# Kernel optimization log

Hardware: AMD Instinct MI355X
Metric: run time of the kernel (lower is better)

## Reference

```python
import jax, jax.numpy as jnp
import numpy as np

N_CLS = 4
NUM_QUERIES = 256
TEMPERATURE = 0.07
NEG_INF = -1e9


def setup_inputs() -> dict:
    key = jax.random.key(0)
    k1, k2, k3, k4, k5, k6 = jax.random.split(key, 6)
    B, C, H, W = 8, 512, 64, 64
    K = 3072
    pred_s = jax.random.normal(k1, (B, N_CLS, H, W), dtype=jnp.float32)
    feat_s_raw = jax.random.normal(k2, (B, C, H, W), dtype=jnp.float32)
    feat_t_raw = jax.random.normal(k3, (B, C, H, W), dtype=jnp.float32)
    target = jax.random.randint(k4, (B, H, W), 0, N_CLS, dtype=jnp.int64)
    queue = jax.random.normal(k5, (C, K), dtype=jnp.float32)
    queue = queue / jnp.linalg.norm(queue, axis=0, keepdims=True)  # F.normalize(queue, dim=0)
    queue_labels = jax.random.randint(k6, (1, K), 0, N_CLS, dtype=jnp.int64)
    return {"pred_s": pred_s, "feat_s_raw": feat_s_raw, "feat_t_raw": feat_t_raw,
            "target": target, "queue": queue, "queue_labels": queue_labels}


def _l2norm(x, axis):
    return x / jnp.clip(jnp.linalg.norm(x, axis=axis, keepdims=True), 1e-12)


def reference(pred_s, feat_s_raw, feat_t_raw, target, queue, queue_labels):
    # softmax over class dim (probs are only consumed in the hard (random=False)
    # branch of find_hard_sampling; module default is random=True)
    probs_s = jax.nn.softmax(pred_s, axis=1)
    fs = _l2norm(feat_s_raw, axis=1)   # [B, C, H, W]
    ft = _l2norm(feat_t_raw, axis=1)
    B, C, H, W = fs.shape

    # permute(0,2,3,1).flatten(0,2) -> [N, C], matching target.reshape(-1)
    rep = jnp.transpose(fs, (0, 2, 3, 1)).reshape(-1, C)
    rep_t = jnp.transpose(ft, (0, 2, 3, 1)).reshape(-1, C)
    tflat = target.reshape(-1)  # [N]

    # find_hard_sampling, random=True path: for each segment, draw NUM_QUERIES
    # indices uniformly from that segment's valid pixels (assumes every class
    # is present, which holds w.h.p. at this resolution).
    key = jax.random.key(42)
    keys = jax.random.split(key, N_CLS + 1)

    def sample_class(k, cls):
        logits = jnp.where(tflat == cls, 0.0, NEG_INF)  # uniform over valid pixels
        return jax.random.categorical(k, logits, shape=(NUM_QUERIES,))

    idx = jax.vmap(sample_class)(keys[:N_CLS], jnp.arange(N_CLS)).reshape(-1)  # [N_CLS*NQ]
    labels = jnp.repeat(jnp.arange(N_CLS), NUM_QUERIES)

    # shuffle (get_shuffle_ids)
    perm = jax.random.permutation(keys[N_CLS], idx.shape[0])
    idx = idx[perm]
    labels = labels[perm]

    feats_s = rep[idx]     # [n, C] random gather (memory-bound)
    feats_t = rep_t[idx]

    l_pos = jnp.einsum('nc,nc->n', feats_s, feats_t)[:, None]   # [n, 1]
    l_neg = jnp.einsum('nc,ck->nk', feats_s, queue)             # [n, K]
    logits = jnp.concatenate([l_pos, l_neg], axis=1) / TEMPERATURE

    # non-targeted mask: eq(labels_cur, queue_labels)
    mask = (labels[:, None] == queue_labels[0][None, :]).astype(logits.dtype)
    return logits, mask, labels
```

## Files before the change

### kernel.cpp

```cpp
#include <hip/hip_runtime.h>
#include <stdint.h>

#define N_PIX   32768
#define C_DIM   512
#define K_Q     3072
#define NCLS    4
#define NQ      256
#define N_SAMP  1024
#define HW      4096
#define L_ROW   3073
#define KH      1024
#define KP      1536

typedef float f32x4 __attribute__((ext_vector_type(4)));
typedef short s16x8 __attribute__((ext_vector_type(8)));

__device__ inline unsigned short f2bf(float f) {
  uint32_t u = __float_as_uint(f);
  return (unsigned short)((u + 0x7FFFu + ((u >> 16) & 1u)) >> 16);
}
__device__ inline float bf2f(unsigned short h) {
  return __uint_as_float(((uint32_t)h) << 16);
}

__host__ __device__ inline void tf2x32(uint32_t k0, uint32_t k1,
                                       uint32_t x0, uint32_t x1,
                                       uint32_t& o0, uint32_t& o1) {
  uint32_t ks2 = k0 ^ k1 ^ 0x1BD11BDAu;
  x0 += k0; x1 += k1;
#define ROTL_(v,d) (((v)<<(d))|((v)>>(32-(d))))
#define RND_(r) { x0 += x1; x1 = ROTL_(x1, r); x1 ^= x0; }
  RND_(13) RND_(15) RND_(26) RND_(6)
  x0 += k1; x1 += ks2 + 1u;
  RND_(17) RND_(29) RND_(16) RND_(24)
  x0 += ks2; x1 += k0 + 2u;
  RND_(13) RND_(15) RND_(26) RND_(6)
  x0 += k0; x1 += k1 + 3u;
  RND_(17) RND_(29) RND_(16) RND_(24)
  x0 += k1; x1 += ks2 + 4u;
  RND_(13) RND_(15) RND_(26) RND_(6)
  x0 += ks2; x1 += k0 + 5u;
  o0 = x0; o1 = x1;
#undef RND_
#undef ROTL_
}

__global__ __launch_bounds__(256) void k_convq(const float* __restrict__ queue,
                                               unsigned short* __restrict__ B2,
                                               int* __restrict__ cnt) {
  if (blockIdx.x == 0 && blockIdx.y == 0 && threadIdx.x < NCLS)
    cnt[threadIdx.x] = 0;
  __shared__ float tile[64][65];
  int tid = threadIdx.x;
  int n0 = blockIdx.x * 64;
  int k0 = blockIdx.y * 64;
#pragma unroll
  for (int it = 0; it < 4; ++it) {
    int r = (tid >> 4) + it * 16;
    int c4 = (tid & 15) * 4;
    float4 v = *(const float4*)(queue + (size_t)(k0 + r) * K_Q + n0 + c4);
    tile[r][c4 + 0] = v.x; tile[r][c4 + 1] = v.y;
    tile[r][c4 + 2] = v.z; tile[r][c4 + 3] = v.w;
  }
  __syncthreads();
  int tn = tid >> 2;
  int kc = (tid & 3) * 16;
  unsigned short* rowp = B2 + (size_t)(n0 + tn) * KH + k0 + kc;
#pragma unroll
  for (int g8 = 0; g8 < 2; ++g8) {
    s16x8 vhi, vlo;
#pragma unroll
    for (int j = 0; j < 8; ++j) {
      float v = tile[kc + g8 * 8 + j][tn];
      unsigned short h = f2bf(v);
      vhi[j] = (short)h;
      vlo[j] = (short)f2bf(v - bf2f(h));
    }
    *(s16x8*)(rowp + g8 * 8)       = vhi;
    *(s16x8*)(rowp + 512 + g8 * 8) = vlo;
  }
}

__global__ __launch_bounds__(256) void k_compact(const int* __restrict__ target,
                                                 int* __restrict__ cnt,
                                                 int* __restrict__ lists) {
  __shared__ int lcnt[NCLS];
  __shared__ int lbase[NCLS];
  int tid = threadIdx.x;
  if (tid < NCLS) lcnt[tid] = 0;
  __syncthreads();
  int p = blockIdx.x * 256 + tid;
  int c = target[p];
  int lpos = atomicAdd(&lcnt[c], 1);
  __syncthreads();
  if (tid < NCLS) lbase[tid] = atomicAdd(&cnt[tid], lcnt[tid]);
  __syncthreads();
  lists[c * N_PIX + lbase[c] + lpos] = p;
}

__global__ __launch_bounds__(256) void k_sample(
    const int* __restrict__ cnt, const int* __restrict__ lists,
    int* __restrict__ samp,
    uint32_t k0a, uint32_t k0b, uint32_t k1a, uint32_t k1b,
    uint32_t k2a, uint32_t k2b, uint32_t k3a, uint32_t k3b) {
  int c = blockIdx.y;
  int q = blockIdx.x;
  uint32_t ka, kb;
  if      (c == 0) { ka = k0a; kb = k0b; }
  else if (c == 1) { ka = k1a; kb = k1b; }
  else if (c == 2) { ka = k2a; kb = k2b; }
  else             { ka = k3a; kb = k3b; }

  int nv = cnt[c];
  const int* lst = lists + c * N_PIX;
  unsigned long long best = 0ull;
  for (int t = threadIdx.x; t < nv; t += 256) {
    int p = lst[t];
    uint32_t j = (uint32_t)(q * N_PIX + p);
    uint32_t o0, o1;
    tf2x32(ka, kb, 0u, j, o0, o1);
    uint32_t bits = o0 ^ o1;
    unsigned long long v =
        ((unsigned long long)(bits >> 9) << 15) | (unsigned)(32767 - p);
    if (v > best) best = v;
  }
  __shared__ unsigned long long red[256];
  red[threadIdx.x] = best;
  __syncthreads();
  for (int s = 128; s > 0; s >>= 1) {
    if (threadIdx.x < s && red[threadIdx.x + s] > red[threadIdx.x])
      red[threadIdx.x] = red[threadIdx.x + s];
    __syncthreads();
  }
  if (threadIdx.x == 0)
    samp[c * NQ + q] = 32767 - (int)(red[0] & 0x7FFFull);
}

__global__ __launch_bounds__(64) void k_perm(
    const int* __restrict__ samp, int* __restrict__ idx_final,
    int* __restrict__ labels_shuf, float* __restrict__ out_labels,
    uint32_t sk0, uint32_t sk1) {
  __shared__ uint32_t keys_s[N_SAMP];
  int lt = threadIdx.x;
  for (int t = lt; t < N_SAMP; t += 64) {
    uint32_t o0, o1;
    tf2x32(sk0, sk1, 0u, (uint32_t)t, o0, o1);
    keys_s[t] = o0 ^ o1;
  }
  __syncthreads();
  int i = blockIdx.x * 64 + lt;
  uint32_t ki = keys_s[i];
  int rank = 0;
#pragma unroll 4
  for (int j = 0; j < N_SAMP; ++j) {
    uint32_t kj = keys_s[j];
    rank += (int)((kj < ki) | ((kj == ki) & (j < i)));
  }
  idx_final[rank] = samp[i];
  int lab = i >> 8;
  labels_shuf[rank] = lab;
  out_labels[rank] = (float)lab;
}

__global__ __launch_bounds__(64) void k_gather(
    const float* __restrict__ fs, const float* __restrict__ ft,
    const int* __restrict__ idx_final, unsigned short* __restrict__ A2,
    float* __restrict__ out_logits) {
  int n = blockIdx.x;
  int p = idx_final[n];
  int b = p >> 12;
  int hw = p & (HW - 1);
  const float* fsb = fs + (size_t)b * C_DIM * HW + hw;
  const float* ftb = ft + (size_t)b * C_DIM * HW + hw;
  int lane = threadIdx.x;

  float s[8], t[8];
#pragma unroll
  for (int j = 0; j < 8; ++j) {
    int c = lane * 8 + j;
    s[j] = fsb[(size_t)c * HW];
    t[j] = ftb[(size_t)c * HW];
  }

  float ss = 0.f, tt = 0.f;
#pragma unroll
  for (int j = 0; j < 8; ++j) { ss += s[j] * s[j]; tt += t[j] * t[j]; }
#pragma unroll
  for (int m = 1; m < 64; m <<= 1) {
    ss += __shfl_xor(ss, m);
    tt += __shfl_xor(tt, m);
  }
  float ns = fmaxf(sqrtf(ss), 1e-12f);
  float nt = fmaxf(sqrtf(tt), 1e-12f);

  float st = 0.f;
  s16x8 vhi, vlo;
#pragma unroll
  for (int j = 0; j < 8; ++j) {
    float a = s[j] / ns;
    float bb = t[j] / nt;
    st += a * bb;
    unsigned short h = f2bf(a);
    vhi[j] = (short)h;
    vlo[j] = (short)f2bf(a - bf2f(h));
  }
  unsigned short* row = A2 + (size_t)n * KH;
  *(s16x8*)(row + lane * 8)       = vhi;
  *(s16x8*)(row + 512 + lane * 8) = vlo;

#pragma unroll
  for (int m = 1; m < 64; m <<= 1) st += __shfl_xor(st, m);
  if (lane == 0)
    out_logits[(size_t)n * L_ROW] = st * (1.0f / 0.07f);
}

__global__ __launch_bounds__(256) void k_gemm(
    const unsigned short* __restrict__ A2,
    const unsigned short* __restrict__ B2,
    const int* __restrict__ labels,
    const int* __restrict__ qlab,
    float* __restrict__ out) {
  __shared__ unsigned short sAB[8192];
  int tid  = threadIdx.x;
  int lane = tid & 63;
  int wave = tid >> 6;
  int wm = wave >> 1, wn = wave & 1;
  int bm = blockIdx.x * 64;
  int bn = blockIdx.y * 64;

  int r0 = tid >> 3;
  int g0 = tid & 7;
  int slot0 = ((g0 ^ (r0 & 7)) << 3);

  f32x4 acc[2][2] = {};
  s16x8 ra[2], rb[2];

  const int NSTEP = KP / 64;
  {
    ra[0] = *(const s16x8*)(A2 + (size_t)(bm + r0)      * KH + g0 * 8);
    ra[1] = *(const s16x8*)(A2 + (size_t)(bm + r0 + 32) * KH + g0 * 8);
    rb[0] = *(const s16x8*)(B2 + (size_t)(bn + r0)      * KH + g0 * 8);
    rb[1] = *(const s16x8*)(B2 + (size_t)(bn + r0 + 32) * KH + g0 * 8);
    *(s16x8*)&sAB[r0 * 64 + slot0]               = ra[0];
    *(s16x8*)&sAB[(r0 + 32) * 64 + slot0]        = ra[1];
    *(s16x8*)&sAB[4096 + r0 * 64 + slot0]        = rb[0];
    *(s16x8*)&sAB[4096 + (r0 + 32) * 64 + slot0] = rb[1];
  }
  __syncthreads();

  for (int s = 0; s < NSTEP; ++s) {
    if (s + 1 < NSTEP) {
      int kp = (s + 1) * 64;
      int sA = (kp < 512) ? kp : kp - 512;
      int sB = (kp < 1024) ? kp : kp - 1024;
      ra[0] = *(const s16x8*)(A2 + (size_t)(bm + r0)      * KH + sA + g0 * 8);
      ra[1] = *(const s16x8*)(A2 + (size_t)(bm + r0 + 32) * KH + sA + g0 * 8);
      rb[0] = *(const s16x8*)(B2 + (size_t)(bn + r0)      * KH + sB + g0 * 8);
      rb[1] = *(const s16x8*)(B2 + (size_t)(bn + r0 + 32) * KH + sB + g0 * 8);
    }
#pragma unroll
    for (int kk = 0; kk < 2; ++kk) {
      int g = kk * 4 + (lane >> 4);
      s16x8 af[2], bfr[2];
#pragma unroll
      for (int mi = 0; mi < 2; ++mi) {
        int rowL = wm * 32 + mi * 16 + (lane & 15);
        af[mi] = *(s16x8*)&sAB[rowL * 64 + ((g ^ (rowL & 7)) << 3)];
      }
#pragma unroll
      for (int ni = 0; ni < 2; ++ni) {
        int rowN = wn * 32 + ni * 16 + (lane & 15);
        bfr[ni] = *(s16x8*)&sAB[4096 + rowN * 64 + ((g ^ (rowN & 7)) << 3)];
      }
#pragma unroll
      for (int mi = 0; mi < 2; ++mi)
#pragma unroll
        for (int ni = 0; ni < 2; ++ni)
          acc[mi][ni] = __builtin_amdgcn_mfma_f32_16x16x32_bf16(
              af[mi], bfr[ni], acc[mi][ni], 0, 0, 0);
    }
    __syncthreads();
    if (s + 1 < NSTEP) {
      *(s16x8*)&sAB[r0 * 64 + slot0]               = ra[0];
      *(s16x8*)&sAB[(r0 + 32) * 64 + slot0]        = ra[1];
      *(s16x8*)&sAB[4096 + r0 * 64 + slot0]        = rb[0];
      *(s16x8*)&sAB[4096 + (r0 + 32) * 64 + slot0] = rb[1];
      __syncthreads();
    }
  }

  int* labsh = (int*)sAB;
  if (tid < 64)            labsh[tid] = labels[bm + tid];
  else if (tid < 128)      labsh[tid] = qlab[bn + (tid - 64)];
  __syncthreads();

  float* out_mask = out + (size_t)N_SAMP * L_ROW;
  const float sc = 1.0f / 0.07f;
#pragma unroll
  for (int mi = 0; mi < 2; ++mi) {
#pragma unroll
    for (int ni = 0; ni < 2; ++ni) {
#pragma unroll
      for (int j = 0; j < 4; ++j) {
        int rl = wm * 32 + mi * 16 + ((lane >> 4) << 2) + j;
        int cl = wn * 32 + ni * 16 + (lane & 15);
        int row = bm + rl, col = bn + cl;
        out[(size_t)row * L_ROW + 1 + col] = acc[mi][ni][j] * sc;
        out_mask[(size_t)row * K_Q + col] =
            (labsh[rl] == labsh[64 + cl]) ? 1.0f : 0.0f;
      }
    }
  }
}

extern "C" void kernel_launch(void* const* d_in, const int* in_sizes, int n_in,
                              void* d_out, int out_size, void* d_ws, size_t ws_size,
                              hipStream_t stream) {
  const float* fs     = (const float*)d_in[1];
  const float* ft     = (const float*)d_in[2];
  const int*   target = (const int*)d_in[3];
  const float* queue  = (const float*)d_in[4];
  const int*   qlab   = (const int*)d_in[5];
  float* out = (float*)d_out;

  char* ws = (char*)d_ws;
  int* cnt   = (int*)(ws + 0);
  int* samp  = (int*)(ws + 4096);
  int* idxf  = (int*)(ws + 8192);
  int* labs  = (int*)(ws + 12288);
  int* lists = (int*)(ws + 16384);
  unsigned short* A2 = (unsigned short*)(ws + (1u << 20));
  unsigned short* B2 = (unsigned short*)(ws + (4u << 20));

  uint32_t ck[5][2];
  for (int i = 0; i < 5; ++i)
    tf2x32(0u, 42u, 0u, (uint32_t)i, ck[i][0], ck[i][1]);
  uint32_t sk0, sk1;
  tf2x32(ck[4][0], ck[4][1], 0u, 1u, sk0, sk1);

  float* out_labels = out + (size_t)N_SAMP * L_ROW + (size_t)N_SAMP * K_Q;

  k_convq<<<dim3(K_Q / 64, C_DIM / 64), 256, 0, stream>>>(queue, B2, cnt);
  k_compact<<<N_PIX / 256, 256, 0, stream>>>(target, cnt, lists);
  k_sample<<<dim3(NQ, NCLS), 256, 0, stream>>>(
      cnt, lists, samp,
      ck[0][0], ck[0][1], ck[1][0], ck[1][1],
      ck[2][0], ck[2][1], ck[3][0], ck[3][1]);
  k_perm<<<16, 64, 0, stream>>>(samp, idxf, labs, out_labels, sk0, sk1);
  k_gather<<<N_SAMP, 64, 0, stream>>>(fs, ft, idxf, A2, out);
  k_gemm<<<dim3(N_SAMP / 64, K_Q / 64), 256, 0, stream>>>(
      A2, B2, labs, qlab, out);
}
```

Measured before the change: 242.9 us.

## Restructure GEMM to single-wave blocks loading MFMA fragments directly from global

```diff
diff --git a/kernel.cpp b/kernel.cpp
--- a/kernel.cpp
+++ b/kernel.cpp
@@ -214,100 +214,81 @@
     out_logits[(size_t)n * L_ROW] = st * (1.0f / 0.07f);
 }
 
-__global__ __launch_bounds__(256) void k_gemm(
+__device__ __forceinline__ void gemm_loadc(
+    const unsigned short* const (&pA)[4], const unsigned short* const (&pB)[4],
+    int sA_, int sB_, s16x8 (&ra)[4], s16x8 (&rb)[4]) {
+  ra[0] = *(const s16x8*)(pA[0] + sA_);
+  ra[1] = *(const s16x8*)(pA[1] + sA_);
+  ra[2] = *(const s16x8*)(pA[2] + sA_);
+  ra[3] = *(const s16x8*)(pA[3] + sA_);
+  rb[0] = *(const s16x8*)(pB[0] + sB_);
+  rb[1] = *(const s16x8*)(pB[1] + sB_);
+  rb[2] = *(const s16x8*)(pB[2] + sB_);
+  rb[3] = *(const s16x8*)(pB[3] + sB_);
+}
+
+__global__ __launch_bounds__(64) void k_gemm(
     const unsigned short* __restrict__ A2,
     const unsigned short* __restrict__ B2,
     const int* __restrict__ labels,
     const int* __restrict__ qlab,
     float* __restrict__ out) {
-  __shared__ unsigned short sAB[8192];
-  int tid  = threadIdx.x;
-  int lane = tid & 63;
-  int wave = tid >> 6;
-  int wm = wave >> 1, wn = wave & 1;
-  int bm = blockIdx.x * 64;
-  int bn = blockIdx.y * 64;
-
-  int r0 = tid >> 3;
-  int g0 = tid & 7;
-  int slot0 = ((g0 ^ (r0 & 7)) << 3);
-
-  f32x4 acc[2][2] = {};
-  s16x8 ra[2], rb[2];
-
-  const int NSTEP = KP / 64;
-  {
-    ra[0] = *(const s16x8*)(A2 + (size_t)(bm + r0)      * KH + g0 * 8);
-    ra[1] = *(const s16x8*)(A2 + (size_t)(bm + r0 + 32) * KH + g0 * 8);
-    rb[0] = *(const s16x8*)(B2 + (size_t)(bn + r0)      * KH + g0 * 8);
-    rb[1] = *(const s16x8*)(B2 + (size_t)(bn + r0 + 32) * KH + g0 * 8);
-    *(s16x8*)&sAB[r0 * 64 + slot0]               = ra[0];
-    *(s16x8*)&sAB[(r0 + 32) * 64 + slot0]        = ra[1];
-    *(s16x8*)&sAB[4096 + r0 * 64 + slot0]        = rb[0];
-    *(s16x8*)&sAB[4096 + (r0 + 32) * 64 + slot0] = rb[1];
-  }
-  __syncthreads();
-
-  for (int s = 0; s < NSTEP; ++s) {
-    if (s + 1 < NSTEP) {
-      int kp = (s + 1) * 64;
-      int sA = (kp < 512) ? kp : kp - 512;
-      int sB = (kp < 1024) ? kp : kp - 1024;
-      ra[0] = *(const s16x8*)(A2 + (size_t)(bm + r0)      * KH + sA + g0 * 8);
-      ra[1] = *(const s16x8*)(A2 + (size_t)(bm + r0 + 32) * KH + sA + g0 * 8);
-      rb[0] = *(const s16x8*)(B2 + (size_t)(bn + r0)      * KH + sB + g0 * 8);
-      rb[1] = *(const s16x8*)(B2 + (size_t)(bn + r0 + 32) * KH + sB + g0 * 8);
+  int lane = threadIdx.x;
+  int bid = (int)blockIdx.x;
+  int swz = (bid & 7) * 96 + (bid >> 3);
+  int bm = (swz & 15) * 64;
+  int bn = (swz >> 4) * 64;
+
+  int koff = (lane >> 4) * 8;
+  int rsel = lane & 15;
+  const unsigned short* pA[4];
+  const unsigned short* pB[4];
+#pragma unroll
+  for (int g = 0; g < 4; ++g) {
+    pA[g] = A2 + (size_t)(bm + g * 16 + rsel) * KH + koff;
+    pB[g] = B2 + (size_t)(bn + g * 16 + rsel) * KH + koff;
+  }
+
+  f32x4 acc[4][4] = {};
+  s16x8 rA[3][4], rB[3][4];
+
+#define SAOF(kp) (((kp) < 512) ? (kp) : (kp) - 512)
+#define SBOF(kp) (((kp) < 1024) ? (kp) : (kp) - 1024)
+
+  gemm_loadc(pA, pB, SAOF(0),  SBOF(0),  rA[0], rB[0]);
+  gemm_loadc(pA, pB, SAOF(32), SBOF(32), rA[1], rB[1]);
+
+#pragma unroll
+  for (int c = 0; c < 48; ++c) {
+    if (c + 2 < 48) {
+      int kp2 = (c + 2) * 32;
+      gemm_loadc(pA, pB, SAOF(kp2), SBOF(kp2), rA[(c + 2) % 3], rB[(c + 2) % 3]);
     }
-#pragma unroll
-    for (int kk = 0; kk < 2; ++kk) {
-      int g = kk * 4 + (lane >> 4);
-      s16x8 af[2], bfr[2];
-#pragma unroll
-      for (int mi = 0; mi < 2; ++mi) {
-        int rowL = wm * 32 + mi * 16 + (lane & 15);
-        af[mi] = *(s16x8*)&sAB[rowL * 64 + ((g ^ (rowL & 7)) << 3)];
-      }
-#pragma unroll
-      for (int ni = 0; ni < 2; ++ni) {
-        int rowN = wn * 32 + ni * 16 + (lane & 15);
-        bfr[ni] = *(s16x8*)&sAB[4096 + rowN * 64 + ((g ^ (rowN & 7)) << 3)];
-      }
-#pragma unroll
-      for (int mi = 0; mi < 2; ++mi)
-#pragma unroll
-        for (int ni = 0; ni < 2; ++ni)
-          acc[mi][ni] = __builtin_amdgcn_mfma_f32_16x16x32_bf16(
-              af[mi], bfr[ni], acc[mi][ni], 0, 0, 0);
-    }
-    __syncthreads();
-    if (s + 1 < NSTEP) {
-      *(s16x8*)&sAB[r0 * 64 + slot0]               = ra[0];
-      *(s16x8*)&sAB[(r0 + 32) * 64 + slot0]        = ra[1];
-      *(s16x8*)&sAB[4096 + r0 * 64 + slot0]        = rb[0];
-      *(s16x8*)&sAB[4096 + (r0 + 32) * 64 + slot0] = rb[1];
-      __syncthreads();
-    }
-  }
-
-  int* labsh = (int*)sAB;
-  if (tid < 64)            labsh[tid] = labels[bm + tid];
-  else if (tid < 128)      labsh[tid] = qlab[bn + (tid - 64)];
-  __syncthreads();
+    int buf = c % 3;
+#pragma unroll
+    for (int mi = 0; mi < 4; ++mi)
+#pragma unroll
+      for (int ni = 0; ni < 4; ++ni)
+        acc[mi][ni] = __builtin_amdgcn_mfma_f32_16x16x32_bf16(
+            rA[buf][mi], rB[buf][ni], acc[mi][ni], 0, 0, 0);
+  }
+#undef SAOF
+#undef SBOF
 
   float* out_mask = out + (size_t)N_SAMP * L_ROW;
   const float sc = 1.0f / 0.07f;
 #pragma unroll
-  for (int mi = 0; mi < 2; ++mi) {
-#pragma unroll
-    for (int ni = 0; ni < 2; ++ni) {
+  for (int mi = 0; mi < 4; ++mi) {
+#pragma unroll
+    for (int ni = 0; ni < 4; ++ni) {
 #pragma unroll
       for (int j = 0; j < 4; ++j) {
-        int rl = wm * 32 + mi * 16 + ((lane >> 4) << 2) + j;
-        int cl = wn * 32 + ni * 16 + (lane & 15);
+        int rl = mi * 16 + ((lane >> 4) << 2) + j;
+        int cl = ni * 16 + (lane & 15);
         int row = bm + rl, col = bn + cl;
         out[(size_t)row * L_ROW + 1 + col] = acc[mi][ni][j] * sc;
         out_mask[(size_t)row * K_Q + col] =
-            (labsh[rl] == labsh[64 + cl]) ? 1.0f : 0.0f;
+            (labels[row] == qlab[col]) ? 1.0f : 0.0f;
       }
     }
   }
@@ -348,6 +329,5 @@
       ck[2][0], ck[2][1], ck[3][0], ck[3][1]);
   k_perm<<<16, 64, 0, stream>>>(samp, idxf, labs, out_labels, sk0, sk1);
   k_gather<<<N_SAMP, 64, 0, stream>>>(fs, ft, idxf, A2, out);
-  k_gemm<<<dim3(N_SAMP / 64, K_Q / 64), 256, 0, stream>>>(
-      A2, B2, labs, qlab, out);
-}
+  k_gemm<<<768, 64, 0, stream>>>(A2, B2, labs, qlab, out);
+}
```

Result: slower. 263.7 us (+8.6%).
